# Kernel optimization log

Measured on AMD Instinct MI355X. Metric: run time of the kernel, lower is better.

## Reference

```python
import jax, jax.numpy as jnp
import numpy as np

B, S, H, I = 2, 2048, 4096, 14336

def setup_inputs() -> dict:
    key = jax.random.key(0)
    k1, k2, k3, k4 = jax.random.split(key, 4)
    sH = 1.0 / np.sqrt(H)
    sI = 1.0 / np.sqrt(I)
    return {
        "x": jax.random.normal(k1, (B, S, H), dtype=jnp.float32),
        "w_gate": jax.random.normal(k2, (I, H), dtype=jnp.float32) * sH,
        "w_up": jax.random.normal(k3, (I, H), dtype=jnp.float32) * sH,
        "w_down": jax.random.normal(k4, (H, I), dtype=jnp.float32) * sI,
    }

def reference(x, w_gate, w_up, w_down):
    # SwiGLU gated MLP: down( silu(x @ Wg^T) * (x @ Wu^T) )
    g = jnp.einsum("bsh,ih->bsi", x, w_gate)   # [B,S,I]
    u = jnp.einsum("bsh,ih->bsi", x, w_up)     # [B,S,I]
    a = jax.nn.silu(g) * u                      # fused silu_mul
    d = jnp.einsum("bsi,hi->bsh", a, w_down)   # [B,S,H]
    return d
```

## Files before the change

kernel.cpp:

```cpp
#include <hip/hip_runtime.h>
#include <hip/hip_bf16.h>
#include <stdint.h>

typedef __bf16 bf16_t;
typedef __bf16 bf16x4 __attribute__((ext_vector_type(4)));
typedef __bf16 bf16x8 __attribute__((ext_vector_type(8)));
typedef float f32x4 __attribute__((ext_vector_type(4)));

#define LDS_CAST(p) ((__attribute__((address_space(3))) void*)(p))
#define GLB_CAST(p) ((const __attribute__((address_space(1))) void*)(p))

__device__ __forceinline__ void gl_lds16(const void* g, void* l) {
  __builtin_amdgcn_global_load_lds(GLB_CAST(g), LDS_CAST(l), 16, 0, 0);
}

#define MFMA16(a,b,c) __builtin_amdgcn_mfma_f32_16x16x32_bf16((a),(b),(c),0,0,0)
#define BARRIER() __builtin_amdgcn_s_barrier()
#define PRIO(n)  __builtin_amdgcn_s_setprio(n)

template<int N> __device__ __forceinline__ void vmw() {
  if constexpr (N == 8)      asm volatile("s_waitcnt vmcnt(8)" ::: "memory");
  else if constexpr (N == 4) asm volatile("s_waitcnt vmcnt(4)" ::: "memory");
  else if constexpr (N == 0) asm volatile("s_waitcnt vmcnt(0)" ::: "memory");
}

static constexpr int M_TOT = 4096, H_DIM = 4096, I_DIM = 14336;

__global__ __launch_bounds__(256)
void k_conv(const float4* __restrict__ src, bf16x4* __restrict__ dst, long n4)
{
  long stride = (long)gridDim.x * blockDim.x;
  for (long i = (long)blockIdx.x * blockDim.x + threadIdx.x; i < n4; i += stride) {
    float4 v = src[i];
    bf16x4 o;
    o[0] = (bf16_t)v.x; o[1] = (bf16_t)v.y; o[2] = (bf16_t)v.z; o[3] = (bf16_t)v.w;
    dst[i] = o;
  }
}

__global__ __launch_bounds__(512, 2)
void k_gateup9(const bf16_t* __restrict__ X, const bf16_t* __restrict__ Wg,
               const bf16_t* __restrict__ Wu, bf16_t* __restrict__ Aout)
{
  __shared__ __align__(1024) char lds[131072];
  const int tid = threadIdx.x, wave = tid >> 6, lane = tid & 63;
  const int lr = lane & 15, kg = lane >> 4;
  const int xm = ((lr >> 3) & 1) << 5;
  const int wm = wave >> 2, wn = wave & 3;
  const int wb = wave * 1024;

  const int bid = blockIdx.x;
  const int bq  = bid >> 3;
  const int tn  = (bid & 7) * 14 + (bq >> 4);
  const int tm  = bq & 15;

  const int srow  = tid >> 2;
  const int scolb = ((tid & 3) * 16) ^ (((tid >> 5) & 1) << 5);

  const bf16_t* gX = X  + (size_t)(tm * 256 + srow) * H_DIM + (scolb >> 1);
  const bf16_t* gG = Wg + (size_t)(tn * 128 + srow) * H_DIM + (scolb >> 1);
  const bf16_t* gU = Wu + (size_t)(tn * 128 + srow) * H_DIM + (scolb >> 1);
  const size_t xh = (size_t)128 * H_DIM;

  const int ck   = (kg * 16) ^ xm;
  const int offA = (wm * 128 + lr) * 64 + ck;
  const int offG = 16384 + (wn * 32 + lr) * 64 + ck;
  const int offU = offG + 8192;

  const f32x4 vz = {0.f, 0.f, 0.f, 0.f};
  f32x4 accg[8][2], accu[8][2];
#pragma unroll
  for (int m = 0; m < 8; ++m)
#pragma unroll
    for (int n = 0; n < 2; ++n) { accg[m][n] = vz; accu[m][n] = vz; }

#define G1_STAGE(TT)                                                         \
  { char* sb = lds + (((TT) & 3) << 15) + wb;                                \
    const int kc = (TT) * 32;                                                \
    gl_lds16(gX + kc,      sb);                                              \
    gl_lds16(gX + xh + kc, sb + 8192);                                       \
    gl_lds16(gG + kc,      sb + 16384);                                      \
    gl_lds16(gU + kc,      sb + 24576); }

#define G1_READS(SET, TT)                                                    \
  { const char* rb = lds + (((TT) & 3) << 15);                               \
    _Pragma("unroll") for (int f = 0; f < 8; ++f)                            \
      a##SET[f] = *(const bf16x8*)(rb + offA + f * 1024);                    \
    _Pragma("unroll") for (int n = 0; n < 2; ++n) {                          \
      bg##SET[n] = *(const bf16x8*)(rb + offG + n * 1024);                   \
      bu##SET[n] = *(const bf16x8*)(rb + offU + n * 1024); } }

#define G1_MFMA(SET)                                                         \
  { PRIO(1);                                                                 \
    _Pragma("unroll") for (int m = 0; m < 8; ++m)                            \
    _Pragma("unroll") for (int n = 0; n < 2; ++n) {                          \
      accg[m][n] = MFMA16(a##SET[m], bg##SET[n], accg[m][n]);                \
      accu[m][n] = MFMA16(a##SET[m], bu##SET[n], accu[m][n]); }              \
    PRIO(0); }

  bf16x8 aA[8], bgA[2], buA[2];
  bf16x8 aB[8], bgB[2], buB[2];

  G1_STAGE(0); G1_STAGE(1); G1_STAGE(2);
  vmw<8>(); BARRIER();
  G1_READS(A, 0);

  const int NT = H_DIM / 32;
  for (int T = 0; T < NT - 4; T += 2) {
    vmw<4>(); BARRIER();
    G1_READS(B, T + 1);
    G1_STAGE(T + 3);
    G1_MFMA(A);
    vmw<4>(); BARRIER();
    G1_READS(A, T + 2);
    G1_STAGE(T + 4);
    G1_MFMA(B);
  }
  vmw<4>(); BARRIER(); G1_READS(B, NT - 3); G1_STAGE(NT - 1); G1_MFMA(A);
  vmw<4>(); BARRIER(); G1_READS(A, NT - 2);                   G1_MFMA(B);
  vmw<0>(); BARRIER(); G1_READS(B, NT - 1);                   G1_MFMA(A);
  G1_MFMA(B);
#undef G1_STAGE
#undef G1_READS
#undef G1_MFMA

  const int r0 = tm * 256 + wm * 128 + kg * 4;
  const int c0 = tn * 128 + wn * 32 + lr;
#pragma unroll
  for (int m = 0; m < 8; ++m)
#pragma unroll
    for (int n = 0; n < 2; ++n)
#pragma unroll
      for (int e = 0; e < 4; ++e) {
        float g = accg[m][n][e];
        float u = accu[m][n][e];
        float s = g / (1.0f + __expf(-g));
        Aout[(size_t)(r0 + m * 16 + e) * I_DIM + c0 + n * 16] = (bf16_t)(s * u);
      }
}

__global__ __launch_bounds__(512, 2)
void k_down9(const bf16_t* __restrict__ Aa, const bf16_t* __restrict__ Wd,
             float* __restrict__ D)
{
  __shared__ __align__(1024) char lds[131072];
  const int tid = threadIdx.x, wave = tid >> 6, lane = tid & 63;
  const int lr = lane & 15, kg = lane >> 4;
  const int xm = ((lr >> 3) & 1) << 5;
  const int wm = wave >> 2, wn = wave & 3;
  const int wb = wave * 1024;

  const int bid = blockIdx.x;
  const int bq  = bid >> 3;
  const int tn  = (bid & 7) * 2 + (bq >> 4);
  const int tm  = bq & 15;

  const int srow  = tid >> 2;
  const int scolb = ((tid & 3) * 16) ^ (((tid >> 5) & 1) << 5);

  const bf16_t* gA = Aa + (size_t)(tm * 256 + srow) * I_DIM + (scolb >> 1);
  const bf16_t* gB = Wd + (size_t)(tn * 256 + srow) * I_DIM + (scolb >> 1);
  const size_t hI = (size_t)128 * I_DIM;

  const int ck   = (kg * 16) ^ xm;
  const int offA = (wm * 128 + lr) * 64 + ck;
  const int offB = 16384 + (wn * 64 + lr) * 64 + ck;

  const f32x4 vz = {0.f, 0.f, 0.f, 0.f};
  f32x4 acc[8][4];
#pragma unroll
  for (int m = 0; m < 8; ++m)
#pragma unroll
    for (int n = 0; n < 4; ++n) acc[m][n] = vz;

#define G2_STAGE(TT)                                                         \
  { char* sb = lds + (((TT) & 3) << 15) + wb;                                \
    const int kc = (TT) * 32;                                                \
    gl_lds16(gA + kc,      sb);                                              \
    gl_lds16(gA + hI + kc, sb + 8192);                                       \
    gl_lds16(gB + kc,      sb + 16384);                                      \
    gl_lds16(gB + hI + kc, sb + 24576); }

#define G2_READS(SET, TT)                                                    \
  { const char* rb = lds + (((TT) & 3) << 15);                               \
    _Pragma("unroll") for (int f = 0; f < 8; ++f)                            \
      a##SET[f] = *(const bf16x8*)(rb + offA + f * 1024);                    \
    _Pragma("unroll") for (int n = 0; n < 4; ++n)                            \
      b##SET[n] = *(const bf16x8*)(rb + offB + n * 1024); }

#define G2_MFMA(SET)                                                         \
  { PRIO(1);                                                                 \
    _Pragma("unroll") for (int m = 0; m < 8; ++m)                            \
    _Pragma("unroll") for (int n = 0; n < 4; ++n)                            \
      acc[m][n] = MFMA16(a##SET[m], b##SET[n], acc[m][n]);                   \
    PRIO(0); }

  bf16x8 aA[8], bA[4];
  bf16x8 aB[8], bB[4];

  G2_STAGE(0); G2_STAGE(1); G2_STAGE(2);
  vmw<8>(); BARRIER();
  G2_READS(A, 0);

  const int NT = I_DIM / 32;
  for (int T = 0; T < NT - 4; T += 2) {
    vmw<4>(); BARRIER();
    G2_READS(B, T + 1);
    G2_STAGE(T + 3);
    G2_MFMA(A);
    vmw<4>(); BARRIER();
    G2_READS(A, T + 2);
    G2_STAGE(T + 4);
    G2_MFMA(B);
  }
  vmw<4>(); BARRIER(); G2_READS(B, NT - 3); G2_STAGE(NT - 1); G2_MFMA(A);
  vmw<4>(); BARRIER(); G2_READS(A, NT - 2);                   G2_MFMA(B);
  vmw<0>(); BARRIER(); G2_READS(B, NT - 1);                   G2_MFMA(A);
  G2_MFMA(B);
#undef G2_STAGE
#undef G2_READS
#undef G2_MFMA

  const int r0 = tm * 256 + wm * 128 + kg * 4;
  const int c0 = tn * 256 + wn * 64 + lr;
#pragma unroll
  for (int m = 0; m < 8; ++m)
#pragma unroll
    for (int n = 0; n < 4; ++n)
#pragma unroll
      for (int e = 0; e < 4; ++e)
        D[(size_t)(r0 + m * 16 + e) * H_DIM + c0 + n * 16] = acc[m][n][e];
}

extern "C" void kernel_launch(void* const* d_in, const int* in_sizes, int n_in,
                              void* d_out, int out_size, void* d_ws, size_t ws_size,
                              hipStream_t stream) {
  const float* x  = (const float*)d_in[0];
  const float* wg = (const float*)d_in[1];
  const float* wu = (const float*)d_in[2];
  const float* wd = (const float*)d_in[3];
  float* out = (float*)d_out;

  const size_t A_BYTES = (size_t)M_TOT * I_DIM * 2;
  const size_t X_BYTES = (size_t)M_TOT * H_DIM * 2;
  const size_t W_BYTES = (size_t)I_DIM * H_DIM * 2;
  char* ws = (char*)d_ws;
  bf16_t* Ab  = (bf16_t*)(ws);
  bf16_t* Xb  = (bf16_t*)(ws + A_BYTES);
  bf16_t* Wgb = (bf16_t*)(ws + A_BYTES + X_BYTES);
  bf16_t* Wub = (bf16_t*)(ws + A_BYTES + X_BYTES + W_BYTES);
  bf16_t* Wdb = Wgb;

  const long nX = (long)M_TOT * H_DIM / 4;
  const long nW = (long)I_DIM * H_DIM / 4;

  k_conv<<<dim3(2048), dim3(256), 0, stream>>>((const float4*)x,  (bf16x4*)Xb,  nX);
  k_conv<<<dim3(2048), dim3(256), 0, stream>>>((const float4*)wg, (bf16x4*)Wgb, nW);
  k_conv<<<dim3(2048), dim3(256), 0, stream>>>((const float4*)wu, (bf16x4*)Wub, nW);

  k_gateup9<<<dim3(16 * 112), dim3(512), 0, stream>>>(Xb, Wgb, Wub, Ab);

  k_conv<<<dim3(2048), dim3(256), 0, stream>>>((const float4*)wd, (bf16x4*)Wdb, nW);

  k_down9<<<dim3(16 * 16), dim3(512), 0, stream>>>(Ab, Wdb, out);
}
```

Baseline: 1.418 ms.

## Restructure down-projection main loop into double-buffered 64-wide K steps with split quarters

Replaces the down-projection kernel's four-stage ring of 32-wide K tiles with a two-buffer scheme of 64-wide K tiles. Each tile is processed in four sub-phases that interleave partial LDS reads, issuance of the next tile's global-to-LDS loads, and 16-MFMA groups. The aim is finer overlap between memory loads and MFMA work and fewer live fragment registers. In exchange it adds more barriers per K step and shallower prefetch depth, which could expose memory latency.

```diff
diff --git a/kernel.cpp b/kernel.cpp
--- a/kernel.cpp
+++ b/kernel.cpp
@@ -16,6 +16,7 @@
 
 #define MFMA16(a,b,c) __builtin_amdgcn_mfma_f32_16x16x32_bf16((a),(b),(c),0,0,0)
 #define BARRIER() __builtin_amdgcn_s_barrier()
+#define LGKM0()  asm volatile("s_waitcnt lgkmcnt(0)" ::: "memory")
 #define PRIO(n)  __builtin_amdgcn_s_setprio(n)
 
 template<int N> __device__ __forceinline__ void vmw() {
@@ -140,8 +141,8 @@
 }
 
 __global__ __launch_bounds__(512, 2)
-void k_down9(const bf16_t* __restrict__ Aa, const bf16_t* __restrict__ Wd,
-             float* __restrict__ D)
+void k_down10(const bf16_t* __restrict__ Aa, const bf16_t* __restrict__ Wd,
+              float* __restrict__ D)
 {
   __shared__ __align__(1024) char lds[131072];
   const int tid = threadIdx.x, wave = tid >> 6, lane = tid & 63;
@@ -164,7 +165,7 @@
 
   const int ck   = (kg * 16) ^ xm;
   const int offA = (wm * 128 + lr) * 64 + ck;
-  const int offB = 16384 + (wn * 64 + lr) * 64 + ck;
+  const int offB = (wn * 64 + lr) * 64 + ck;
 
   const f32x4 vz = {0.f, 0.f, 0.f, 0.f};
   f32x4 acc[8][4];
@@ -173,53 +174,128 @@
 #pragma unroll
     for (int n = 0; n < 4; ++n) acc[m][n] = vz;
 
-#define G2_STAGE(TT)                                                         \
-  { char* sb = lds + (((TT) & 3) << 15) + wb;                                \
-    const int kc = (TT) * 32;                                                \
-    gl_lds16(gA + kc,      sb);                                              \
-    gl_lds16(gA + hI + kc, sb + 8192);                                       \
-    gl_lds16(gB + kc,      sb + 16384);                                      \
-    gl_lds16(gB + hI + kc, sb + 24576); }
-
-#define G2_READS(SET, TT)                                                    \
-  { const char* rb = lds + (((TT) & 3) << 15);                               \
-    _Pragma("unroll") for (int f = 0; f < 8; ++f)                            \
-      a##SET[f] = *(const bf16x8*)(rb + offA + f * 1024);                    \
-    _Pragma("unroll") for (int n = 0; n < 4; ++n)                            \
-      b##SET[n] = *(const bf16x8*)(rb + offB + n * 1024); }
-
-#define G2_MFMA(SET)                                                         \
-  { PRIO(1);                                                                 \
-    _Pragma("unroll") for (int m = 0; m < 8; ++m)                            \
-    _Pragma("unroll") for (int n = 0; n < 4; ++n)                            \
-      acc[m][n] = MFMA16(a##SET[m], b##SET[n], acc[m][n]);                   \
-    PRIO(0); }
-
-  bf16x8 aA[8], bA[4];
-  bf16x8 aB[8], bB[4];
-
-  G2_STAGE(0); G2_STAGE(1); G2_STAGE(2);
-  vmw<8>(); BARRIER();
-  G2_READS(A, 0);
-
-  const int NT = I_DIM / 32;
-  for (int T = 0; T < NT - 4; T += 2) {
-    vmw<4>(); BARRIER();
-    G2_READS(B, T + 1);
-    G2_STAGE(T + 3);
-    G2_MFMA(A);
-    vmw<4>(); BARRIER();
-    G2_READS(A, T + 2);
-    G2_STAGE(T + 4);
-    G2_MFMA(B);
+  gl_lds16(gA,           lds + 0     + wb);
+  gl_lds16(gA + hI,      lds + 8192  + wb);
+  gl_lds16(gB,           lds + 32768 + wb);
+  gl_lds16(gB + hI,      lds + 40960 + wb);
+  gl_lds16(gA + 32,      lds + 16384 + wb);
+  gl_lds16(gA + hI + 32, lds + 24576 + wb);
+  gl_lds16(gB + 32,      lds + 49152 + wb);
+  gl_lds16(gB + hI + 32, lds + 57344 + wb);
+  vmw<4>(); BARRIER();
+
+  const int NT = I_DIM / 64;
+  for (int T = 0; T <= NT - 2; ++T) {
+    const char* bb = lds + (T & 1) * 65536;
+    char* sb = lds + ((T + 1) & 1) * 65536 + wb;
+    const bf16_t* gAn = gA + (T + 1) * 64;
+    const bf16_t* gBn = gB + (T + 1) * 64;
+    bf16x8 bv[4];
+    {
+      bf16x8 a[4];
+#pragma unroll
+      for (int f = 0; f < 4; ++f) a[f] = *(const bf16x8*)(bb + offA + f * 1024);
+#pragma unroll
+      for (int n = 0; n < 4; ++n) bv[n] = *(const bf16x8*)(bb + 32768 + offB + n * 1024);
+      gl_lds16(gAn, sb); gl_lds16(gAn + hI, sb + 8192);
+      BARRIER(); LGKM0();
+      PRIO(1);
+#pragma unroll
+      for (int m = 0; m < 4; ++m)
+#pragma unroll
+        for (int n = 0; n < 4; ++n) acc[m][n] = MFMA16(a[m], bv[n], acc[m][n]);
+      PRIO(0);
+      BARRIER();
+    }
+    {
+      bf16x8 a[4];
+#pragma unroll
+      for (int f = 0; f < 4; ++f) a[f] = *(const bf16x8*)(bb + offA + (f + 4) * 1024);
+      gl_lds16(gBn, sb + 32768); gl_lds16(gBn + hI, sb + 40960);
+      BARRIER(); LGKM0();
+      PRIO(1);
+#pragma unroll
+      for (int m = 0; m < 4; ++m)
+#pragma unroll
+        for (int n = 0; n < 4; ++n) acc[4 + m][n] = MFMA16(a[m], bv[n], acc[4 + m][n]);
+      PRIO(0);
+      vmw<4>(); BARRIER();
+    }
+    {
+      bf16x8 a[4];
+#pragma unroll
+      for (int f = 0; f < 4; ++f) a[f] = *(const bf16x8*)(bb + 16384 + offA + f * 1024);
+#pragma unroll
+      for (int n = 0; n < 4; ++n) bv[n] = *(const bf16x8*)(bb + 49152 + offB + n * 1024);
+      gl_lds16(gAn + 32, sb + 16384); gl_lds16(gAn + hI + 32, sb + 24576);
+      BARRIER(); LGKM0();
+      PRIO(1);
+#pragma unroll
+      for (int m = 0; m < 4; ++m)
+#pragma unroll
+        for (int n = 0; n < 4; ++n) acc[m][n] = MFMA16(a[m], bv[n], acc[m][n]);
+      PRIO(0);
+      BARRIER();
+    }
+    {
+      bf16x8 a[4];
+#pragma unroll
+      for (int f = 0; f < 4; ++f) a[f] = *(const bf16x8*)(bb + 16384 + offA + (f + 4) * 1024);
+      gl_lds16(gBn + 32, sb + 49152); gl_lds16(gBn + hI + 32, sb + 57344);
+      BARRIER(); LGKM0();
+      PRIO(1);
+#pragma unroll
+      for (int m = 0; m < 4; ++m)
+#pragma unroll
+        for (int n = 0; n < 4; ++n) acc[4 + m][n] = MFMA16(a[m], bv[n], acc[4 + m][n]);
+      PRIO(0);
+      vmw<4>(); BARRIER();
+    }
   }
-  vmw<4>(); BARRIER(); G2_READS(B, NT - 3); G2_STAGE(NT - 1); G2_MFMA(A);
-  vmw<4>(); BARRIER(); G2_READS(A, NT - 2);                   G2_MFMA(B);
-  vmw<0>(); BARRIER(); G2_READS(B, NT - 1);                   G2_MFMA(A);
-  G2_MFMA(B);
-#undef G2_STAGE
-#undef G2_READS
-#undef G2_MFMA
+  {
+    const char* bb = lds + ((NT - 1) & 1) * 65536;
+    bf16x8 bv[4];
+    { bf16x8 a[4];
+#pragma unroll
+      for (int f = 0; f < 4; ++f) a[f] = *(const bf16x8*)(bb + offA + f * 1024);
+#pragma unroll
+      for (int n = 0; n < 4; ++n) bv[n] = *(const bf16x8*)(bb + 32768 + offB + n * 1024);
+      BARRIER(); LGKM0(); PRIO(1);
+#pragma unroll
+      for (int m = 0; m < 4; ++m)
+#pragma unroll
+        for (int n = 0; n < 4; ++n) acc[m][n] = MFMA16(a[m], bv[n], acc[m][n]);
+      PRIO(0); BARRIER(); }
+    { bf16x8 a[4];
+#pragma unroll
+      for (int f = 0; f < 4; ++f) a[f] = *(const bf16x8*)(bb + offA + (f + 4) * 1024);
+      BARRIER(); LGKM0(); PRIO(1);
+#pragma unroll
+      for (int m = 0; m < 4; ++m)
+#pragma unroll
+        for (int n = 0; n < 4; ++n) acc[4 + m][n] = MFMA16(a[m], bv[n], acc[4 + m][n]);
+      PRIO(0); vmw<0>(); BARRIER(); }
+    { bf16x8 a[4];
+#pragma unroll
+      for (int f = 0; f < 4; ++f) a[f] = *(const bf16x8*)(bb + 16384 + offA + f * 1024);
+#pragma unroll
+      for (int n = 0; n < 4; ++n) bv[n] = *(const bf16x8*)(bb + 49152 + offB + n * 1024);
+      LGKM0(); PRIO(1);
+#pragma unroll
+      for (int m = 0; m < 4; ++m)
+#pragma unroll
+        for (int n = 0; n < 4; ++n) acc[m][n] = MFMA16(a[m], bv[n], acc[m][n]);
+      PRIO(0); }
+    { bf16x8 a[4];
+#pragma unroll
+      for (int f = 0; f < 4; ++f) a[f] = *(const bf16x8*)(bb + 16384 + offA + (f + 4) * 1024);
+      LGKM0(); PRIO(1);
+#pragma unroll
+      for (int m = 0; m < 4; ++m)
+#pragma unroll
+        for (int n = 0; n < 4; ++n) acc[4 + m][n] = MFMA16(a[m], bv[n], acc[4 + m][n]);
+      PRIO(0); }
+  }
 
   const int r0 = tm * 256 + wm * 128 + kg * 4;
   const int c0 = tn * 256 + wn * 64 + lr;
@@ -262,5 +338,5 @@
 
   k_conv<<<dim3(2048), dim3(256), 0, stream>>>((const float4*)wd, (bf16x4*)Wdb, nW);
 
-  k_down9<<<dim3(16 * 16), dim3(512), 0, stream>>>(Ab, Wdb, out);
-}
+  k_down10<<<dim3(16 * 16), dim3(512), 0, stream>>>(Ab, Wdb, out);
+}
```

Result: no change. 1.436 ms (+1.3%).
